# Optimization experiments

Measured on AMD Instinct MI355X. Metric: run time of the kernel, lower is better.

The kernel has to match this reference:

```python
import jax, jax.numpy as jnp
import numpy as np

N_NODES = 50000
N_EDGES = 800000
D = 96
DEPTH = 2


def setup_inputs() -> dict:
    key = jax.random.key(0)
    ks = jax.random.split(key, 8)
    scale = 1.0 / np.sqrt(D)
    x = jax.random.normal(ks[0], (N_NODES, D), dtype=jnp.float32)
    W0 = jax.random.normal(ks[1], (DEPTH, D, D), dtype=jnp.float32) * scale
    b0 = jnp.zeros((DEPTH, D), dtype=jnp.float32)
    W1 = jax.random.normal(ks[2], (DEPTH, D, D), dtype=jnp.float32) * scale
    b1 = jnp.zeros((DEPTH, D), dtype=jnp.float32)
    W2 = jax.random.normal(ks[3], (DEPTH, 2 * D, D), dtype=jnp.float32) * (1.0 / np.sqrt(2 * D))
    b2 = jnp.zeros((DEPTH, D), dtype=jnp.float32)
    edge_src = jax.random.randint(ks[4], (N_EDGES,), 0, N_NODES, dtype=jnp.int64 if jax.config.jax_enable_x64 else jnp.int32)
    edge_dst = jnp.sort(jax.random.randint(ks[5], (N_EDGES,), 0, N_NODES, dtype=jnp.int64 if jax.config.jax_enable_x64 else jnp.int32))
    return {"x": x, "W0": W0, "b0": b0, "W1": W1, "b1": b1,
            "W2": W2, "b2": b2, "edge_src": edge_src, "edge_dst": edge_dst}


def reference(x, W0, b0, W1, b1, W2, b2, edge_src, edge_dst):
    # x: [N, D] node features; edge lists define sparse adjacency A (A[dst, src] = 1).
    n = x.shape[0]
    depth = W0.shape[0]
    for i in range(depth):
        h_self = x @ W1[i] + b1[i]                      # [N, D] self transform
        h_nb = x @ W0[i] + b0[i]                        # [N, D] neighbor transform
        # sparse.mm(A, h_nb): sum of h_nb over in-neighbors of each vertex
        agg = jax.ops.segment_sum(h_nb[edge_src], edge_dst, num_segments=n)  # [N, D]
        x = jnp.concatenate([h_self, agg], axis=-1) @ W2[i] + b2[i]          # [N, D]
        # torch.std uses unbiased estimator (ddof=1)
        x = x / jnp.std(x, axis=-1, ddof=1, keepdims=True)
    return x
```

## Files before the change

kernel.cpp:

```cpp
#include <hip/hip_runtime.h>
#include <hip/hip_bf16.h>

typedef __attribute__((ext_vector_type(8))) short short8;
typedef __attribute__((ext_vector_type(16))) float f32x16;

__device__ __forceinline__ float bf2f(unsigned short h){
  union{unsigned u; float f;} c; c.u = ((unsigned)h)<<16; return c.f;
}
__device__ __forceinline__ unsigned short f2bf(float f){
  union{float f; unsigned u;} c; c.f = f;
  return (unsigned short)((c.u + 0x7fffu + ((c.u>>16)&1u))>>16);
}


__global__ __launch_bounds__(256) void k_pre(
    const float* __restrict__ x,  const float* __restrict__ W0,
    const float* __restrict__ W1, const float* __restrict__ W2,
    const float* __restrict__ b0, const float* __restrict__ b1,
    const float* __restrict__ b2, const int* __restrict__ dst,
    unsigned short* __restrict__ WcF, float* __restrict__ cvec,
    float* __restrict__ dvec, unsigned short* __restrict__ xb,
    unsigned short* __restrict__ xf, int* __restrict__ rs,
    int nN, int nE, int depth, int castBlocks)
{
  const int b = blockIdx.x, tid = threadIdx.x;
  const int nwc = depth*192;
  if (b < nwc){
    __shared__ float sm[96];
    int i = b/192, k = b%192;
    float s = 0.f;
    if (tid < 192){
      int c = tid % 96, jh = tid / 96;
      const float* w  = (k<96) ? (W1 + (size_t)i*9216 + (size_t)k*96)
                               : (W0 + (size_t)i*9216 + (size_t)(k-96)*96);
      const float* w2 = W2 + (size_t)i*18432 + (k<96 ? 0 : 9216);
      int j0 = jh*48;
      float s0=0.f,s1=0.f,s2=0.f,s3=0.f;
      for (int j=j0;j<j0+48;j+=4){
        s0 += w[j]   * w2[(j)*96 + c];
        s1 += w[j+1] * w2[(j+1)*96 + c];
        s2 += w[j+2] * w2[(j+2)*96 + c];
        s3 += w[j+3] * w2[(j+3)*96 + c];
      }
      s = (s0+s1)+(s2+s3);
      if (jh==1) sm[c] = s;
    }
    __syncthreads();
    if (tid < 96){
      float tot = s + sm[tid];
      int kt=k>>4, hfk=(k>>3)&1, jj=k&7;
      int t=tid>>5, cl=tid&31;
      WcF[(size_t)((i*12+kt)*3+t)*512 + (size_t)(hfk*32+cl)*8 + jj] = f2bf(tot);
    }
  } else if (b < nwc + depth){
    int i = b - nwc;
    if (tid < 96){
      const float* w2 = W2 + (size_t)i*18432;
      float s = b2[i*96+tid], d=0.f;
      for (int j=0;j<96;++j){
        s += b1[i*96+j]*w2[j*96+tid];
        d += b0[i*96+j]*w2[(96+j)*96+tid];
      }
      cvec[i*96+tid]=s; dvec[i*96+tid]=d;
    }
  } else if (b < nwc + depth + castBlocks){
    int t2 = (b - nwc - depth)*256 + tid;
    if (t2 >= nN*12) return;
    int n = t2/12, q = t2%12;
    const float4* src = reinterpret_cast<const float4*>(x + (size_t)n*96 + q*8);
    float4 f0 = src[0], f1 = src[1];
    uint4 o;
    o.x = (unsigned)f2bf(f0.x) | ((unsigned)f2bf(f0.y)<<16);
    o.y = (unsigned)f2bf(f0.z) | ((unsigned)f2bf(f0.w)<<16);
    o.z = (unsigned)f2bf(f1.x) | ((unsigned)f2bf(f1.y)<<16);
    o.w = (unsigned)f2bf(f1.z) | ((unsigned)f2bf(f1.w)<<16);
    *reinterpret_cast<uint4*>(xb + (size_t)n*96 + q*8) = o;
    int strip=n>>5, cl=n&31, kt=q>>1, hf=q&1;
    *reinterpret_cast<uint4*>(xf + ((size_t)(strip*6+kt)*64 + hf*32+cl)*8) = o;
  } else {
    int n = (b - nwc - depth - castBlocks)*256 + tid;
    if (n > nN) return;
    int lo=0, hi=nE;
    while(lo<hi){int mid=(lo+hi)>>1; if(dst[mid]<n) lo=mid+1; else hi=mid;}
    rs[n]=lo;
  }
}

__device__ __forceinline__ void acc8(float* a, uint4 v){
  a[0] += bf2f((unsigned short)(v.x & 0xffffu));
  a[1] += bf2f((unsigned short)(v.x >> 16));
  a[2] += bf2f((unsigned short)(v.y & 0xffffu));
  a[3] += bf2f((unsigned short)(v.y >> 16));
  a[4] += bf2f((unsigned short)(v.z & 0xffffu));
  a[5] += bf2f((unsigned short)(v.z >> 16));
  a[6] += bf2f((unsigned short)(v.w & 0xffffu));
  a[7] += bf2f((unsigned short)(v.w >> 16));
}

__global__ __launch_bounds__(192) void k_agg(
    const unsigned short* __restrict__ xb, const int* __restrict__ esrc,
    const int* __restrict__ rs, unsigned short* __restrict__ xaf,
    int* __restrict__ deg, int nN)
{
  int n = blockIdx.x*16 + threadIdx.y;
  if (n >= nN) return;
  const int q = threadIdx.x;
  const unsigned short* xq = xb + q*8;
  const int e0 = rs[n], e1 = rs[n+1];
  if (q == 0) deg[n] = e1 - e0;

  float a[8] = {0,0,0,0,0,0,0,0};

  int e = e0;
  for (; e+8 <= e1; e += 8){
    int s0 = esrc[e],   s1 = esrc[e+1], s2 = esrc[e+2], s3 = esrc[e+3];
    int s4 = esrc[e+4], s5 = esrc[e+5], s6 = esrc[e+6], s7 = esrc[e+7];
    uint4 v0 = *reinterpret_cast<const uint4*>(xq + (size_t)s0*96);
    uint4 v1 = *reinterpret_cast<const uint4*>(xq + (size_t)s1*96);
    uint4 v2 = *reinterpret_cast<const uint4*>(xq + (size_t)s2*96);
    uint4 v3 = *reinterpret_cast<const uint4*>(xq + (size_t)s3*96);
    uint4 v4 = *reinterpret_cast<const uint4*>(xq + (size_t)s4*96);
    uint4 v5 = *reinterpret_cast<const uint4*>(xq + (size_t)s5*96);
    uint4 v6 = *reinterpret_cast<const uint4*>(xq + (size_t)s6*96);
    uint4 v7 = *reinterpret_cast<const uint4*>(xq + (size_t)s7*96);
    acc8(a, v0); acc8(a, v1); acc8(a, v2); acc8(a, v3);
    acc8(a, v4); acc8(a, v5); acc8(a, v6); acc8(a, v7);
  }
  for (; e+4 <= e1; e += 4){
    int s0 = esrc[e], s1 = esrc[e+1], s2 = esrc[e+2], s3 = esrc[e+3];
    uint4 v0 = *reinterpret_cast<const uint4*>(xq + (size_t)s0*96);
    uint4 v1 = *reinterpret_cast<const uint4*>(xq + (size_t)s1*96);
    uint4 v2 = *reinterpret_cast<const uint4*>(xq + (size_t)s2*96);
    uint4 v3 = *reinterpret_cast<const uint4*>(xq + (size_t)s3*96);
    acc8(a, v0); acc8(a, v1); acc8(a, v2); acc8(a, v3);
  }
  for (; e < e1; ++e){
    int s = esrc[e];
    uint4 v = *reinterpret_cast<const uint4*>(xq + (size_t)s*96);
    acc8(a, v);
  }

  uint4 o;
  o.x = (unsigned)f2bf(a[0]) | ((unsigned)f2bf(a[1]) << 16);
  o.y = (unsigned)f2bf(a[2]) | ((unsigned)f2bf(a[3]) << 16);
  o.z = (unsigned)f2bf(a[4]) | ((unsigned)f2bf(a[5]) << 16);
  o.w = (unsigned)f2bf(a[6]) | ((unsigned)f2bf(a[7]) << 16);
  int strip=n>>5, cl=n&31, kt=q>>1, hf=q&1;
  *reinterpret_cast<uint4*>(xaf + ((size_t)(strip*6+kt)*64 + hf*32+cl)*8) = o;
}

template<int LAST>
__global__ __launch_bounds__(256) void k_gemm(
    const unsigned short* __restrict__ xf, const unsigned short* __restrict__ xaf,
    const unsigned short* __restrict__ WcF, const float* __restrict__ cvec,
    const float* __restrict__ dvec, const int* __restrict__ deg,
    float* __restrict__ outf, unsigned short* __restrict__ outb,
    unsigned short* __restrict__ xfo, int nN)
{
  const int wid = (blockIdx.x<<2) + (threadIdx.x>>6);
  const int nstrips = (nN+31)>>5;
  if (wid >= nstrips) return;
  const int lane = threadIdx.x & 63;
  const int cl = lane & 31;
  const int hf = lane >> 5;
  const int row0 = wid << 5;

  const short8* xfp = reinterpret_cast<const short8*>(xf)  + (size_t)wid*6*64;
  const short8* xap = reinterpret_cast<const short8*>(xaf) + (size_t)wid*6*64;
  const short8* wf  = reinterpret_cast<const short8*>(WcF);

  short8 afr[12];
  #pragma unroll
  for (int kt=0; kt<6; ++kt){ afr[kt] = xfp[kt*64 + lane]; afr[6+kt] = xap[kt*64 + lane]; }

  f32x16 acc[3];
  #pragma unroll
  for (int t=0;t<3;++t){
    #pragma unroll
    for (int i=0;i<16;++i) acc[t][i] = 0.f;
  }

  #pragma unroll
  for (int kt=0; kt<12; ++kt){
    short8 a = afr[kt];
    #pragma unroll
    for (int t=0;t<3;++t){
      short8 b = wf[(kt*3+t)*64 + lane];
      acc[t] = __builtin_amdgcn_mfma_f32_32x32x16_bf16(a, b, acc[t], 0, 0, 0);
    }
  }

  float cv[3], dv[3];
  #pragma unroll
  for (int t=0;t<3;++t){ cv[t] = cvec[t*32+cl]; dv[t] = dvec[t*32+cl]; }

  const int jj  = cl & 7;
  const int hfd = (cl >> 3) & 1;
  const int ktb = cl >> 4;

  #pragma unroll
  for (int r=0;r<16;++r){
    const int rl = (r&3) + ((r>>2)<<3) + (hf<<2);
    const int rg = row0 + rl;
    const int rgc = rg < nN ? rg : nN-1;
    const float dgv = (float)deg[rgc];
    float v0 = acc[0][r] + cv[0] + dgv*dv[0];
    float v1 = acc[1][r] + cv[1] + dgv*dv[1];
    float v2 = acc[2][r] + cv[2] + dgv*dv[2];
    float s  = v0+v1+v2;
    float s2 = v0*v0 + v1*v1 + v2*v2;
    #pragma unroll
    for (int m=1;m<32;m<<=1){ s += __shfl_xor(s,m,64); s2 += __shfl_xor(s2,m,64); }
    float var = (s2 - s*s*(1.0f/96.0f)) * (1.0f/95.0f);
    float sc  = 1.0f / sqrtf(var);
    if (rg < nN){
      if (LAST){
        float* o = outf + (size_t)rg*96;
        o[cl] = v0*sc; o[32+cl] = v1*sc; o[64+cl] = v2*sc;
      } else {
        unsigned short h0 = f2bf(v0*sc), h1 = f2bf(v1*sc), h2 = f2bf(v2*sc);
        unsigned short* o = outb + (size_t)rg*96;
        o[cl] = h0; o[32+cl] = h1; o[64+cl] = h2;
        size_t base = (size_t)wid*3072 + (size_t)(hfd*32 + rl)*8 + jj;
        xfo[base + (size_t)(ktb  )*512] = h0;
        xfo[base + (size_t)(ktb+2)*512] = h1;
        xfo[base + (size_t)(ktb+4)*512] = h2;
      }
    }
  }
}

extern "C" void kernel_launch(void* const* d_in, const int* in_sizes, int n_in,
                              void* d_out, int out_size, void* d_ws, size_t ws_size,
                              hipStream_t stream)
{
  const float* x   = (const float*)d_in[0];
  const float* W0  = (const float*)d_in[1];
  const float* b0  = (const float*)d_in[2];
  const float* W1  = (const float*)d_in[3];
  const float* b1  = (const float*)d_in[4];
  const float* W2  = (const float*)d_in[5];
  const float* b2  = (const float*)d_in[6];
  const int* esrc  = (const int*)d_in[7];
  const int* edst  = (const int*)d_in[8];
  const int nN = in_sizes[0] / 96;
  const int nE = in_sizes[7];
  const int depth = in_sizes[1] / (96*96);
  float* out = (float*)d_out;

  const int nstrips = (nN+31)/32;

  char* p = (char*)d_ws;
  auto alloc = [&](size_t bytes)->char*{ char* r = p; p += (bytes + 255) & ~(size_t)255; return r; };
  unsigned short* WcF  = (unsigned short*)alloc((size_t)depth*12*3*512*2);
  float* cvec          = (float*)alloc((size_t)depth*96*4);
  float* dvec          = (float*)alloc((size_t)depth*96*4);
  int* rs              = (int*)alloc((size_t)(nN+1)*4);
  int* deg             = (int*)alloc((size_t)nN*4);
  unsigned short* xb0  = (unsigned short*)alloc((size_t)nN*96*2);
  unsigned short* xb1  = (unsigned short*)alloc((size_t)nN*96*2);
  unsigned short* xf   = (unsigned short*)alloc((size_t)nstrips*3072*2);
  unsigned short* xaf  = (unsigned short*)alloc((size_t)nstrips*3072*2);

  const int castBlocks = (nN*12+255)/256;
  const int rpBlocks   = (nN+1+255)/256;
  const int preGrid    = depth*192 + depth + castBlocks + rpBlocks;
  k_pre<<<dim3(preGrid), dim3(256), 0, stream>>>(
      x, W0, W1, W2, b0, b1, b2, edst, WcF, cvec, dvec, xb0, xf, rs,
      nN, nE, depth, castBlocks);

  const int aggGrid  = (nN+15)/16;
  const int gemmGrid = (nstrips+3)/4;

  unsigned short* cur = xb0;
  unsigned short* nxt = xb1;
  for (int i=0; i<depth; ++i){
    k_agg<<<dim3(aggGrid), dim3(12,16), 0, stream>>>(cur, esrc, rs, xaf, deg, nN);
    if (i == depth-1){
      k_gemm<1><<<dim3(gemmGrid), dim3(256), 0, stream>>>(
          xf, xaf, WcF + (size_t)i*12*3*512, cvec + i*96, dvec + i*96, deg,
          out, (unsigned short*)nullptr, (unsigned short*)nullptr, nN);
    } else {
      k_gemm<0><<<dim3(gemmGrid), dim3(256), 0, stream>>>(
          xf, xaf, WcF + (size_t)i*12*3*512, cvec + i*96, dvec + i*96, deg,
          (float*)nullptr, nxt, xf, nN);
      unsigned short* t = cur; cur = nxt; nxt = t;
    }
  }
}
```

Before: 177.8 us.

## Fuse neighbor aggregation into the MFMA GEMM kernel via LDS staging

Merges the separate aggregation and GEMM kernels into one kernel per layer. Each 384-thread block gathers and sums neighbor features for a 32-node strip, with edge indices staged through LDS in chunks. It writes the aggregated bf16 tile to LDS in MFMA fragment layout, and one wave then runs the GEMM plus normalization. This removes the global write and reread of the aggregated buffer, the degree array and one launch per layer. In exchange, five of six waves sit idle during the GEMM tail, and the block adds extra barriers.

```diff
diff --git a/kernel.cpp b/kernel.cpp
--- a/kernel.cpp
+++ b/kernel.cpp
@@ -97,81 +97,97 @@
   a[7] += bf2f((unsigned short)(v.w >> 16));
 }
 
-__global__ __launch_bounds__(192) void k_agg(
-    const unsigned short* __restrict__ xb, const int* __restrict__ esrc,
-    const int* __restrict__ rs, unsigned short* __restrict__ xaf,
-    int* __restrict__ deg, int nN)
-{
-  int n = blockIdx.x*16 + threadIdx.y;
-  if (n >= nN) return;
-  const int q = threadIdx.x;
-  const unsigned short* xq = xb + q*8;
-  const int e0 = rs[n], e1 = rs[n+1];
-  if (q == 0) deg[n] = e1 - e0;
-
-  float a[8] = {0,0,0,0,0,0,0,0};
-
-  int e = e0;
-  for (; e+8 <= e1; e += 8){
-    int s0 = esrc[e],   s1 = esrc[e+1], s2 = esrc[e+2], s3 = esrc[e+3];
-    int s4 = esrc[e+4], s5 = esrc[e+5], s6 = esrc[e+6], s7 = esrc[e+7];
-    uint4 v0 = *reinterpret_cast<const uint4*>(xq + (size_t)s0*96);
-    uint4 v1 = *reinterpret_cast<const uint4*>(xq + (size_t)s1*96);
-    uint4 v2 = *reinterpret_cast<const uint4*>(xq + (size_t)s2*96);
-    uint4 v3 = *reinterpret_cast<const uint4*>(xq + (size_t)s3*96);
-    uint4 v4 = *reinterpret_cast<const uint4*>(xq + (size_t)s4*96);
-    uint4 v5 = *reinterpret_cast<const uint4*>(xq + (size_t)s5*96);
-    uint4 v6 = *reinterpret_cast<const uint4*>(xq + (size_t)s6*96);
-    uint4 v7 = *reinterpret_cast<const uint4*>(xq + (size_t)s7*96);
-    acc8(a, v0); acc8(a, v1); acc8(a, v2); acc8(a, v3);
-    acc8(a, v4); acc8(a, v5); acc8(a, v6); acc8(a, v7);
-  }
-  for (; e+4 <= e1; e += 4){
-    int s0 = esrc[e], s1 = esrc[e+1], s2 = esrc[e+2], s3 = esrc[e+3];
-    uint4 v0 = *reinterpret_cast<const uint4*>(xq + (size_t)s0*96);
-    uint4 v1 = *reinterpret_cast<const uint4*>(xq + (size_t)s1*96);
-    uint4 v2 = *reinterpret_cast<const uint4*>(xq + (size_t)s2*96);
-    uint4 v3 = *reinterpret_cast<const uint4*>(xq + (size_t)s3*96);
-    acc8(a, v0); acc8(a, v1); acc8(a, v2); acc8(a, v3);
-  }
-  for (; e < e1; ++e){
-    int s = esrc[e];
-    uint4 v = *reinterpret_cast<const uint4*>(xq + (size_t)s*96);
-    acc8(a, v);
-  }
-
-  uint4 o;
-  o.x = (unsigned)f2bf(a[0]) | ((unsigned)f2bf(a[1]) << 16);
-  o.y = (unsigned)f2bf(a[2]) | ((unsigned)f2bf(a[3]) << 16);
-  o.z = (unsigned)f2bf(a[4]) | ((unsigned)f2bf(a[5]) << 16);
-  o.w = (unsigned)f2bf(a[6]) | ((unsigned)f2bf(a[7]) << 16);
-  int strip=n>>5, cl=n&31, kt=q>>1, hf=q&1;
-  *reinterpret_cast<uint4*>(xaf + ((size_t)(strip*6+kt)*64 + hf*32+cl)*8) = o;
-}
-
+#define ECAP 2048
 template<int LAST>
-__global__ __launch_bounds__(256) void k_gemm(
-    const unsigned short* __restrict__ xf, const unsigned short* __restrict__ xaf,
+__global__ __launch_bounds__(384) void k_fused(
+    const unsigned short* __restrict__ xb, const unsigned short* __restrict__ xf,
+    const int* __restrict__ esrc, const int* __restrict__ rs,
     const unsigned short* __restrict__ WcF, const float* __restrict__ cvec,
-    const float* __restrict__ dvec, const int* __restrict__ deg,
+    const float* __restrict__ dvec,
     float* __restrict__ outf, unsigned short* __restrict__ outb,
     unsigned short* __restrict__ xfo, int nN)
 {
-  const int wid = (blockIdx.x<<2) + (threadIdx.x>>6);
-  const int nstrips = (nN+31)>>5;
-  if (wid >= nstrips) return;
-  const int lane = threadIdx.x & 63;
+  __shared__ short aL[6*64*8];
+  __shared__ int   eL[ECAP];
+  __shared__ int   rsL[33];
+
+  const int tid = threadIdx.x;
+  const int wid = blockIdx.x;
+  const int row0 = wid << 5;
+
+  if (tid < 33){
+    int nidx = row0 + tid; if (nidx > nN) nidx = nN;
+    rsL[tid] = rs[nidx];
+  }
+  __syncthreads();
+  const int base = rsL[0];
+  const int cnt  = rsL[32] - base;
+
+  const int nl = tid / 12;
+  const int q  = tid - nl*12;
+  const unsigned short* xq = xb + q*8;
+  const int e0 = rsL[nl], e1 = rsL[nl+1];
+  float a[8] = {0,0,0,0,0,0,0,0};
+
+  for (int cb = base; cb < base + cnt; cb += ECAP){
+    const int clen = min(ECAP, base + cnt - cb);
+    if (cb != base) __syncthreads();
+    for (int i = tid; i < clen; i += 384) eL[i] = esrc[cb + i];
+    __syncthreads();
+    int e  = max(e0, cb);
+    int hi = min(e1, cb + clen);
+    const int* ep = eL - cb;
+    for (; e+8 <= hi; e += 8){
+      int s0=ep[e],s1=ep[e+1],s2=ep[e+2],s3=ep[e+3];
+      int s4=ep[e+4],s5=ep[e+5],s6=ep[e+6],s7=ep[e+7];
+      uint4 v0=*reinterpret_cast<const uint4*>(xq+(size_t)s0*96);
+      uint4 v1=*reinterpret_cast<const uint4*>(xq+(size_t)s1*96);
+      uint4 v2=*reinterpret_cast<const uint4*>(xq+(size_t)s2*96);
+      uint4 v3=*reinterpret_cast<const uint4*>(xq+(size_t)s3*96);
+      uint4 v4=*reinterpret_cast<const uint4*>(xq+(size_t)s4*96);
+      uint4 v5=*reinterpret_cast<const uint4*>(xq+(size_t)s5*96);
+      uint4 v6=*reinterpret_cast<const uint4*>(xq+(size_t)s6*96);
+      uint4 v7=*reinterpret_cast<const uint4*>(xq+(size_t)s7*96);
+      acc8(a,v0); acc8(a,v1); acc8(a,v2); acc8(a,v3);
+      acc8(a,v4); acc8(a,v5); acc8(a,v6); acc8(a,v7);
+    }
+    for (; e+4 <= hi; e += 4){
+      int s0=ep[e],s1=ep[e+1],s2=ep[e+2],s3=ep[e+3];
+      uint4 v0=*reinterpret_cast<const uint4*>(xq+(size_t)s0*96);
+      uint4 v1=*reinterpret_cast<const uint4*>(xq+(size_t)s1*96);
+      uint4 v2=*reinterpret_cast<const uint4*>(xq+(size_t)s2*96);
+      uint4 v3=*reinterpret_cast<const uint4*>(xq+(size_t)s3*96);
+      acc8(a,v0); acc8(a,v1); acc8(a,v2); acc8(a,v3);
+    }
+    for (; e < hi; ++e){
+      uint4 v=*reinterpret_cast<const uint4*>(xq+(size_t)ep[e]*96);
+      acc8(a,v);
+    }
+  }
+
+  {
+    uint4 o;
+    o.x=(unsigned)f2bf(a[0])|((unsigned)f2bf(a[1])<<16);
+    o.y=(unsigned)f2bf(a[2])|((unsigned)f2bf(a[3])<<16);
+    o.z=(unsigned)f2bf(a[4])|((unsigned)f2bf(a[5])<<16);
+    o.w=(unsigned)f2bf(a[6])|((unsigned)f2bf(a[7])<<16);
+    *reinterpret_cast<uint4*>(&aL[((q>>1)*64 + (q&1)*32 + nl)<<3]) = o;
+  }
+  __syncthreads();
+
+  if (tid >= 64) return;
+
+  const int lane = tid;
   const int cl = lane & 31;
   const int hf = lane >> 5;
-  const int row0 = wid << 5;
-
-  const short8* xfp = reinterpret_cast<const short8*>(xf)  + (size_t)wid*6*64;
-  const short8* xap = reinterpret_cast<const short8*>(xaf) + (size_t)wid*6*64;
+
+  const short8* xfp = reinterpret_cast<const short8*>(xf) + (size_t)wid*384;
+  const short8* aLs = reinterpret_cast<const short8*>(aL);
   const short8* wf  = reinterpret_cast<const short8*>(WcF);
 
-  short8 afr[12];
-  #pragma unroll
-  for (int kt=0; kt<6; ++kt){ afr[kt] = xfp[kt*64 + lane]; afr[6+kt] = xap[kt*64 + lane]; }
+  short8 afr[6];
+  #pragma unroll
+  for (int kt=0; kt<6; ++kt) afr[kt] = xfp[kt*64 + lane];
 
   f32x16 acc[3];
   #pragma unroll
@@ -182,11 +198,11 @@
 
   #pragma unroll
   for (int kt=0; kt<12; ++kt){
-    short8 a = afr[kt];
+    short8 av = (kt < 6) ? afr[kt] : aLs[(kt-6)*64 + lane];
     #pragma unroll
     for (int t=0;t<3;++t){
       short8 b = wf[(kt*3+t)*64 + lane];
-      acc[t] = __builtin_amdgcn_mfma_f32_32x32x16_bf16(a, b, acc[t], 0, 0, 0);
+      acc[t] = __builtin_amdgcn_mfma_f32_32x32x16_bf16(av, b, acc[t], 0, 0, 0);
     }
   }
 
@@ -202,8 +218,7 @@
   for (int r=0;r<16;++r){
     const int rl = (r&3) + ((r>>2)<<3) + (hf<<2);
     const int rg = row0 + rl;
-    const int rgc = rg < nN ? rg : nN-1;
-    const float dgv = (float)deg[rgc];
+    const float dgv = (float)(rsL[rl+1] - rsL[rl]);
     float v0 = acc[0][r] + cv[0] + dgv*dv[0];
     float v1 = acc[1][r] + cv[1] + dgv*dv[1];
     float v2 = acc[2][r] + cv[2] + dgv*dv[2];
@@ -221,10 +236,10 @@
         unsigned short h0 = f2bf(v0*sc), h1 = f2bf(v1*sc), h2 = f2bf(v2*sc);
         unsigned short* o = outb + (size_t)rg*96;
         o[cl] = h0; o[32+cl] = h1; o[64+cl] = h2;
-        size_t base = (size_t)wid*3072 + (size_t)(hfd*32 + rl)*8 + jj;
-        xfo[base + (size_t)(ktb  )*512] = h0;
-        xfo[base + (size_t)(ktb+2)*512] = h1;
-        xfo[base + (size_t)(ktb+4)*512] = h2;
+        size_t bofs = (size_t)wid*3072 + (size_t)(hfd*32 + rl)*8 + jj;
+        xfo[bofs + (size_t)(ktb  )*512] = h0;
+        xfo[bofs + (size_t)(ktb+2)*512] = h1;
+        xfo[bofs + (size_t)(ktb+4)*512] = h2;
       }
     }
   }
@@ -256,11 +271,9 @@
   float* cvec          = (float*)alloc((size_t)depth*96*4);
   float* dvec          = (float*)alloc((size_t)depth*96*4);
   int* rs              = (int*)alloc((size_t)(nN+1)*4);
-  int* deg             = (int*)alloc((size_t)nN*4);
   unsigned short* xb0  = (unsigned short*)alloc((size_t)nN*96*2);
   unsigned short* xb1  = (unsigned short*)alloc((size_t)nN*96*2);
   unsigned short* xf   = (unsigned short*)alloc((size_t)nstrips*3072*2);
-  unsigned short* xaf  = (unsigned short*)alloc((size_t)nstrips*3072*2);
 
   const int castBlocks = (nN*12+255)/256;
   const int rpBlocks   = (nN+1+255)/256;
@@ -269,20 +282,16 @@
       x, W0, W1, W2, b0, b1, b2, edst, WcF, cvec, dvec, xb0, xf, rs,
       nN, nE, depth, castBlocks);
 
-  const int aggGrid  = (nN+15)/16;
-  const int gemmGrid = (nstrips+3)/4;
-
   unsigned short* cur = xb0;
   unsigned short* nxt = xb1;
   for (int i=0; i<depth; ++i){
-    k_agg<<<dim3(aggGrid), dim3(12,16), 0, stream>>>(cur, esrc, rs, xaf, deg, nN);
     if (i == depth-1){
-      k_gemm<1><<<dim3(gemmGrid), dim3(256), 0, stream>>>(
-          xf, xaf, WcF + (size_t)i*12*3*512, cvec + i*96, dvec + i*96, deg,
+      k_fused<1><<<dim3(nstrips), dim3(384), 0, stream>>>(
+          cur, xf, esrc, rs, WcF + (size_t)i*12*3*512, cvec + i*96, dvec + i*96,
           out, (unsigned short*)nullptr, (unsigned short*)nullptr, nN);
     } else {
-      k_gemm<0><<<dim3(gemmGrid), dim3(256), 0, stream>>>(
-          xf, xaf, WcF + (size_t)i*12*3*512, cvec + i*96, dvec + i*96, deg,
+      k_fused<0><<<dim3(nstrips), dim3(384), 0, stream>>>(
+          cur, xf, esrc, rs, WcF + (size_t)i*12*3*512, cvec + i*96, dvec + i*96,
           (float*)nullptr, nxt, xf, nN);
       unsigned short* t = cur; cur = nxt; nxt = t;
     }
```

New measurement: 171.1 us. 1.04x faster.
